# Kernel optimization log

Measured on AMD Instinct MI355X. Metric: run time of the kernel, lower is better.

Reference implementation:

```python
import jax, jax.numpy as jnp
import numpy as np

INPUT_DIM = 2048
N_EXPERTS = 64
K = 2


def setup_inputs() -> dict:
    key = jax.random.key(0)
    kx, kw, kb = jax.random.split(key, 3)
    x = jax.random.normal(kx, (4, 4096, INPUT_DIM), dtype=jnp.float32)
    # nn.Linear(input_dim, n_experts): weight [n_experts, input_dim], bias [n_experts]
    bound = 1.0 / np.sqrt(INPUT_DIM)
    W = jax.random.uniform(kw, (N_EXPERTS, INPUT_DIM), minval=-bound, maxval=bound, dtype=jnp.float32)
    b = jax.random.uniform(kb, (N_EXPERTS,), minval=-bound, maxval=bound, dtype=jnp.float32)
    return {"x": x, "W": W, "b": b}


def reference(x, W, b):
    # logits: [B, S, E]
    logits = jnp.einsum('bsd,ed->bse', x, W) + b
    topk_vals, topk_indices = jax.lax.top_k(logits, K)  # over last (expert) axis
    gate_probs = jax.nn.softmax(topk_vals, axis=-1)
    return gate_probs, topk_indices
```

## Files before the change

kernel.cpp:

```cpp
#include <hip/hip_runtime.h>
#include <math.h>
#include <stdint.h>

typedef _Float16 half8 __attribute__((ext_vector_type(8)));
typedef float floatx4 __attribute__((ext_vector_type(4)));

#define NTOK 16384
#define DIM  2048
#define NEXP 64
#define MB   32
#define NBLK (NTOK / MB)
#define THREADS 512
#define WSW_H8 16384
#define WSW_BYTES (2 * WSW_H8 * 16)

__global__ void wprep_kernel(const float* __restrict__ W, _Float16* __restrict__ wsw) {
    const int id   = blockIdx.x * blockDim.x + threadIdx.x;
    const int lane = id & 63;
    const int tg   = (id >> 6) & 3;
    const int sg   = id >> 8;
    const int e    = tg * 16 + (lane & 15);
    const int k    = sg * 32 + (lane >> 4) * 8;
    const float* src = W + (size_t)e * DIM + k;
    half8 h, l;
#pragma unroll
    for (int j = 0; j < 8; j++) {
        const float v  = src[j];
        const _Float16 hh = (_Float16)v;
        h[j] = hh;
        l[j] = (_Float16)((v - (float)hh) * 2048.0f);
    }
    const size_t slot = (size_t)(sg * 4 + tg) * 64 + lane;
    ((half8*)wsw)[slot]          = h;
    ((half8*)wsw)[WSW_H8 + slot] = l;
}

__device__ __forceinline__ void split_a(const float4& v0, const float4& v1,
                                        half8& hi, half8& lo) {
    const float av[8] = {v0.x, v0.y, v0.z, v0.w, v1.x, v1.y, v1.z, v1.w};
#pragma unroll
    for (int j = 0; j < 8; j++) {
        const _Float16 hh = (_Float16)av[j];
        hi[j] = hh;
        lo[j] = (_Float16)((av[j] - (float)hh) * 2048.0f);
    }
}

template <bool USE_WS>
__global__ __launch_bounds__(THREADS, 2)
void gating_regB_kernel(const float* __restrict__ x, const float* __restrict__ W,
                        const _Float16* __restrict__ wsw, const float* __restrict__ bias,
                        float* __restrict__ out)
{
    __shared__ __align__(16) float part[8 * MB * 64];

    const int tid  = threadIdx.x;
    const int lane = tid & 63;
    const int w    = tid >> 6;
    const int col  = lane & 15;
    const int quad = lane >> 4;
    const int tok0 = blockIdx.x * MB;
    const int sg0  = w * 8;

    floatx4 accm[2][4], accl[2][4];
#pragma unroll
    for (int m = 0; m < 2; m++)
#pragma unroll
        for (int tg = 0; tg < 4; tg++) { accm[m][tg] = {0,0,0,0}; accl[m][tg] = {0,0,0,0}; }

    const half8* bb    = (const half8*)wsw + lane;
    const float* xbase = x + (size_t)tok0 * DIM + quad * 8;

    for (int ss = 0; ss < 4; ++ss) {
        const int sgA = sg0 + 2 * ss;

        half8 bh[2][4], bl[2][4];
        if constexpr (USE_WS) {
#pragma unroll
            for (int s2 = 0; s2 < 2; ++s2)
#pragma unroll
                for (int tg = 0; tg < 4; ++tg) {
                    const size_t fi = (size_t)((sgA + s2) * 4 + tg) * 64;
                    bh[s2][tg] = bb[fi];
                    bl[s2][tg] = bb[WSW_H8 + fi];
                }
        } else {
#pragma unroll
            for (int s2 = 0; s2 < 2; ++s2)
#pragma unroll
                for (int tg = 0; tg < 4; ++tg) {
                    const float* wr = W + (size_t)(tg * 16 + col) * DIM + (sgA + s2) * 32 + quad * 8;
                    split_a(*(const float4*)wr, *(const float4*)(wr + 4), bh[s2][tg], bl[s2][tg]);
                }
        }
        float4 av[2][2][2];
#pragma unroll
        for (int m = 0; m < 2; ++m)
#pragma unroll
            for (int s2 = 0; s2 < 2; ++s2) {
                const float* ap = xbase + (size_t)(m * 16 + col) * DIM + (sgA + s2) * 32;
                av[m][s2][0] = *(const float4*)(ap);
                av[m][s2][1] = *(const float4*)(ap + 4);
            }

        __builtin_amdgcn_sched_barrier(0);

#pragma unroll
        for (int m = 0; m < 2; ++m)
#pragma unroll
            for (int s2 = 0; s2 < 2; ++s2) {
                half8 ah, al;
                split_a(av[m][s2][0], av[m][s2][1], ah, al);
#pragma unroll
                for (int tg = 0; tg < 4; ++tg) {
                    accm[m][tg] = __builtin_amdgcn_mfma_f32_16x16x32_f16(ah, bh[s2][tg], accm[m][tg], 0, 0, 0);
                    accl[m][tg] = __builtin_amdgcn_mfma_f32_16x16x32_f16(ah, bl[s2][tg], accl[m][tg], 0, 0, 0);
                    accl[m][tg] = __builtin_amdgcn_mfma_f32_16x16x32_f16(al, bh[s2][tg], accl[m][tg], 0, 0, 0);
                }
            }
    }

    const float inv = 1.0f / 2048.0f;
#pragma unroll
    for (int m = 0; m < 2; ++m)
#pragma unroll
        for (int tg = 0; tg < 4; ++tg)
#pragma unroll
            for (int r = 0; r < 4; ++r)
                part[w * 2048 + (m * 16 + quad * 4 + r) * 64 + tg * 16 + col]
                    = accm[m][tg][r] + accl[m][tg][r] * inv;
    __syncthreads();

    floatx4 red = {0, 0, 0, 0};
#pragma unroll
    for (int w2 = 0; w2 < 8; ++w2)
        red += *(const floatx4*)(part + w2 * 2048 + tid * 4);
    const floatx4 bv = *(const floatx4*)(bias + ((tid * 4) & 63));
    __syncthreads();

    float* fin = part;
#pragma unroll
    for (int i = 0; i < 4; ++i) {
        const int p = tid * 4 + i;
        fin[(p >> 6) * 65 + (p & 63)] = red[i] + bv[i];
    }
    __syncthreads();

    if (tid < MB) {
        const int t = tid;
        float v0 = -INFINITY, v1 = -INFINITY;
        int   i0 = 0, i1 = 0;
        for (int e = 0; e < NEXP; e++) {
            const float v = fin[t * 65 + e];
            if (v > v0) { v1 = v0; i1 = i0; v0 = v; i0 = e; }
            else if (v > v1) { v1 = v; i1 = e; }
        }
        const float e1 = expf(v1 - v0);
        const float sden = 1.f + e1;
        const int   g  = tok0 + t;
        out[2 * g + 0] = 1.f / sden;
        out[2 * g + 1] = e1 / sden;
        out[2 * NTOK + 2 * g + 0] = (float)i0;
        out[2 * NTOK + 2 * g + 1] = (float)i1;
    }
}

extern "C" void kernel_launch(void* const* d_in, const int* in_sizes, int n_in,
                              void* d_out, int out_size, void* d_ws, size_t ws_size,
                              hipStream_t stream) {
    const float* x    = (const float*)d_in[0];
    const float* W    = (const float*)d_in[1];
    const float* bias = (const float*)d_in[2];
    float*       out  = (float*)d_out;
    _Float16*    wsw  = (_Float16*)d_ws;

    if (ws_size >= (size_t)WSW_BYTES) {
        hipLaunchKernelGGL(wprep_kernel, dim3(64), dim3(256), 0, stream, (const float*)d_in[1], wsw);
        hipLaunchKernelGGL((gating_regB_kernel<true>), dim3(NBLK), dim3(THREADS), 0, stream,
                           x, W, wsw, bias, out);
    } else {
        hipLaunchKernelGGL((gating_regB_kernel<false>), dim3(NBLK), dim3(THREADS), 0, stream,
                           x, W, wsw, bias, out);
    }
}
```

Measured before the change: 213.2 us.

## Shrink gating tiles to 16 tokens with 4-way K split per block

Each block now handles 16 tokens with 256 threads, and the four waves each take a quarter of the K dimension. This replaces 32 tokens per block across 8 waves with register-held two-step B fragments. The change lowers register pressure, allows more resident blocks per CU and gives finer load balance, with the aim of hiding memory latency better for this bandwidth-bound x read. The cost is that each B (weight) fragment is reused across only 16 tokens instead of 32, which doubles weight-fragment loads per token. The explicit batched-load prefetch scheduling is also dropped.

Result: no change. 215.9 us (+1.3%).

```diff
diff --git a/kernel.cpp b/kernel.cpp
--- a/kernel.cpp
+++ b/kernel.cpp
@@ -8,9 +8,11 @@
 #define NTOK 16384
 #define DIM  2048
 #define NEXP 64
-#define MB   32
-#define NBLK (NTOK / MB)
-#define THREADS 512
+#define TPW  16
+#define KSPLIT 4
+#define KSLICE (DIM / KSPLIT)
+#define NSTEP  (KSLICE / 32)
+#define NBLK (NTOK / TPW)
 #define WSW_H8 16384
 #define WSW_BYTES (2 * WSW_H8 * 16)
 
@@ -47,94 +49,64 @@
 }
 
 template <bool USE_WS>
-__global__ __launch_bounds__(THREADS, 2)
-void gating_regB_kernel(const float* __restrict__ x, const float* __restrict__ W,
+__global__ __launch_bounds__(256, 4)
+void gating_lean_kernel(const float* __restrict__ x, const float* __restrict__ W,
                         const _Float16* __restrict__ wsw, const float* __restrict__ bias,
                         float* __restrict__ out)
 {
-    __shared__ __align__(16) float part[8 * MB * 64];
+    __shared__ __align__(16) float part[KSPLIT * TPW * NEXP];
 
     const int tid  = threadIdx.x;
     const int lane = tid & 63;
     const int w    = tid >> 6;
     const int col  = lane & 15;
     const int quad = lane >> 4;
-    const int tok0 = blockIdx.x * MB;
-    const int sg0  = w * 8;
+    const int tok0 = blockIdx.x * TPW;
 
-    floatx4 accm[2][4], accl[2][4];
+    floatx4 accm[4] = {{0,0,0,0},{0,0,0,0},{0,0,0,0},{0,0,0,0}};
+    floatx4 accl[4] = {{0,0,0,0},{0,0,0,0},{0,0,0,0},{0,0,0,0}};
+
+    const float* xrow = x + (size_t)(tok0 + col) * DIM + w * KSLICE + quad * 8;
+    const half8* bb   = (const half8*)wsw + lane;
+
+#pragma unroll 2
+    for (int s = 0; s < NSTEP; ++s) {
+        const float4 v0 = *(const float4*)(xrow + s * 32);
+        const float4 v1 = *(const float4*)(xrow + s * 32 + 4);
+        half8 ah, al;
+        split_a(v0, v1, ah, al);
+
+        const int sg = w * NSTEP + s;
 #pragma unroll
-    for (int m = 0; m < 2; m++)
-#pragma unroll
-        for (int tg = 0; tg < 4; tg++) { accm[m][tg] = {0,0,0,0}; accl[m][tg] = {0,0,0,0}; }
-
-    const half8* bb    = (const half8*)wsw + lane;
-    const float* xbase = x + (size_t)tok0 * DIM + quad * 8;
-
-    for (int ss = 0; ss < 4; ++ss) {
-        const int sgA = sg0 + 2 * ss;
-
-        half8 bh[2][4], bl[2][4];
-        if constexpr (USE_WS) {
-#pragma unroll
-            for (int s2 = 0; s2 < 2; ++s2)
-#pragma unroll
-                for (int tg = 0; tg < 4; ++tg) {
-                    const size_t fi = (size_t)((sgA + s2) * 4 + tg) * 64;
-                    bh[s2][tg] = bb[fi];
-                    bl[s2][tg] = bb[WSW_H8 + fi];
-                }
-        } else {
-#pragma unroll
-            for (int s2 = 0; s2 < 2; ++s2)
-#pragma unroll
-                for (int tg = 0; tg < 4; ++tg) {
-                    const float* wr = W + (size_t)(tg * 16 + col) * DIM + (sgA + s2) * 32 + quad * 8;
-                    split_a(*(const float4*)wr, *(const float4*)(wr + 4), bh[s2][tg], bl[s2][tg]);
-                }
+        for (int tg = 0; tg < 4; ++tg) {
+            half8 bh, bl;
+            if constexpr (USE_WS) {
+                const size_t fi = (size_t)(sg * 4 + tg) * 64;
+                bh = bb[fi];
+                bl = bb[WSW_H8 + fi];
+            } else {
+                const float* wr = W + (size_t)(tg * 16 + col) * DIM + sg * 32 + quad * 8;
+                split_a(*(const float4*)wr, *(const float4*)(wr + 4), bh, bl);
+            }
+            accm[tg] = __builtin_amdgcn_mfma_f32_16x16x32_f16(ah, bh, accm[tg], 0, 0, 0);
+            accl[tg] = __builtin_amdgcn_mfma_f32_16x16x32_f16(ah, bl, accl[tg], 0, 0, 0);
+            accl[tg] = __builtin_amdgcn_mfma_f32_16x16x32_f16(al, bh, accl[tg], 0, 0, 0);
         }
-        float4 av[2][2][2];
-#pragma unroll
-        for (int m = 0; m < 2; ++m)
-#pragma unroll
-            for (int s2 = 0; s2 < 2; ++s2) {
-                const float* ap = xbase + (size_t)(m * 16 + col) * DIM + (sgA + s2) * 32;
-                av[m][s2][0] = *(const float4*)(ap);
-                av[m][s2][1] = *(const float4*)(ap + 4);
-            }
-
-        __builtin_amdgcn_sched_barrier(0);
-
-#pragma unroll
-        for (int m = 0; m < 2; ++m)
-#pragma unroll
-            for (int s2 = 0; s2 < 2; ++s2) {
-                half8 ah, al;
-                split_a(av[m][s2][0], av[m][s2][1], ah, al);
-#pragma unroll
-                for (int tg = 0; tg < 4; ++tg) {
-                    accm[m][tg] = __builtin_amdgcn_mfma_f32_16x16x32_f16(ah, bh[s2][tg], accm[m][tg], 0, 0, 0);
-                    accl[m][tg] = __builtin_amdgcn_mfma_f32_16x16x32_f16(ah, bl[s2][tg], accl[m][tg], 0, 0, 0);
-                    accl[m][tg] = __builtin_amdgcn_mfma_f32_16x16x32_f16(al, bh[s2][tg], accl[m][tg], 0, 0, 0);
-                }
-            }
     }
 
     const float inv = 1.0f / 2048.0f;
 #pragma unroll
-    for (int m = 0; m < 2; ++m)
+    for (int tg = 0; tg < 4; ++tg)
 #pragma unroll
-        for (int tg = 0; tg < 4; ++tg)
-#pragma unroll
-            for (int r = 0; r < 4; ++r)
-                part[w * 2048 + (m * 16 + quad * 4 + r) * 64 + tg * 16 + col]
-                    = accm[m][tg][r] + accl[m][tg][r] * inv;
+        for (int r = 0; r < 4; ++r)
+            part[w * (TPW * NEXP) + (quad * 4 + r) * NEXP + tg * 16 + col]
+                = accm[tg][r] + accl[tg][r] * inv;
     __syncthreads();
 
     floatx4 red = {0, 0, 0, 0};
 #pragma unroll
-    for (int w2 = 0; w2 < 8; ++w2)
-        red += *(const floatx4*)(part + w2 * 2048 + tid * 4);
+    for (int w2 = 0; w2 < KSPLIT; ++w2)
+        red += *(const floatx4*)(part + w2 * (TPW * NEXP) + tid * 4);
     const floatx4 bv = *(const floatx4*)(bias + ((tid * 4) & 63));
     __syncthreads();
 
@@ -146,7 +118,7 @@
     }
     __syncthreads();
 
-    if (tid < MB) {
+    if (tid < TPW) {
         const int t = tid;
         float v0 = -INFINITY, v1 = -INFINITY;
         int   i0 = 0, i1 = 0;
@@ -176,10 +148,10 @@
 
     if (ws_size >= (size_t)WSW_BYTES) {
         hipLaunchKernelGGL(wprep_kernel, dim3(64), dim3(256), 0, stream, (const float*)d_in[1], wsw);
-        hipLaunchKernelGGL((gating_regB_kernel<true>), dim3(NBLK), dim3(THREADS), 0, stream,
+        hipLaunchKernelGGL((gating_lean_kernel<true>), dim3(NBLK), dim3(256), 0, stream,
                            x, W, wsw, bias, out);
     } else {
-        hipLaunchKernelGGL((gating_regB_kernel<false>), dim3(NBLK), dim3(THREADS), 0, stream,
+        hipLaunchKernelGGL((gating_lean_kernel<false>), dim3(NBLK), dim3(256), 0, stream,
                            x, W, wsw, bias, out);
     }
 }
```
